# Kernel optimization log

Measured on AMD Instinct MI355X. Metric: run time of the kernel, lower is better.

The kernel has to match this reference:

```python
import jax, jax.numpy as jnp
import numpy as np

H = 16
D_MODEL = 1024
D_K = D_MODEL // H
SEQ = 2048
BATCH = 2


def setup_inputs() -> dict:
    key = jax.random.key(0)
    ks = jax.random.split(key, 11)
    s = 1.0 / np.sqrt(D_MODEL)
    inp = {
        "query": jax.random.normal(ks[0], (SEQ, BATCH, D_MODEL), jnp.float32),
        "key_": jax.random.normal(ks[1], (SEQ, BATCH, D_MODEL), jnp.float32),
        "value": jax.random.normal(ks[2], (SEQ, BATCH, D_MODEL), jnp.float32),
        "Wq": jax.random.uniform(ks[3], (D_MODEL, D_MODEL), jnp.float32, -s, s),
        "bq": jax.random.uniform(ks[4], (D_MODEL,), jnp.float32, -s, s),
        "Wk": jax.random.uniform(ks[5], (D_MODEL, D_MODEL), jnp.float32, -s, s),
        "bk": jax.random.uniform(ks[6], (D_MODEL,), jnp.float32, -s, s),
        "Wv": jax.random.uniform(ks[7], (D_MODEL, D_MODEL), jnp.float32, -s, s),
        "bv": jax.random.uniform(ks[8], (D_MODEL,), jnp.float32, -s, s),
        "Wo": jax.random.uniform(ks[9], (D_MODEL, D_MODEL), jnp.float32, -s, s),
        "bo": jax.random.uniform(ks[10], (D_MODEL,), jnp.float32, -s, s),
    }
    return inp


def _mha(query, key_, value, Wq, bq, Wk, bk, Wv, bv, Wo, bo):
    S, B, D = query.shape
    # torch Linear: x @ W.T + b; then view(S,B,h,dk).transpose(0,2) -> [h,B,S,dk]
    def proj(x, W, b):
        return jnp.transpose((x @ W.T + b).reshape(S, B, H, D_K), (2, 1, 0, 3))

    q = proj(query, Wq, bq)   # [h, b, S, dk]
    k = proj(key_, Wk, bk)
    v = proj(value, Wv, bv)

    scores = jnp.einsum("hbqd,hbkd->hbqk", q, k) / jnp.sqrt(
        jnp.asarray(D_K, q.dtype)
    )  # [h, b, S, S]
    p_attn = jax.nn.softmax(scores, axis=-1)  # dropout p=0.0 -> identity
    x = jnp.einsum("hbqk,hbkd->hbqd", p_attn, v)  # [h, b, S, dk]
    x = jnp.transpose(x, (2, 1, 0, 3)).reshape(S, B, D)  # back to [S, B, D]
    return x @ Wo.T + bo


def reference(query, key_, value, Wq, bq, Wk, bk, Wv, bv, Wo, bo):
    return _mha(query, key_, value, Wq, bq, Wk, bk, Wv, bv, Wo, bo)
```

## Files before the change

### kernel.cpp

```cpp
#include <hip/hip_runtime.h>

#define SEQ   2048
#define BATCH 2
#define DM    1024
#define NH    16
#define DKD   64
#define MROWS (SEQ*BATCH)

#define QSCALE 0.18033688011112042f

using bf16x8 = __attribute__((ext_vector_type(8))) __bf16;
using bf16x4 = __attribute__((ext_vector_type(4))) __bf16;
using bf16x2 = __attribute__((ext_vector_type(2))) __bf16;
using f32x4  = __attribute__((ext_vector_type(4))) float;

__device__ __forceinline__ void gld_lds16(const __bf16* g, __bf16* l) {
  __builtin_amdgcn_global_load_lds(
      (__attribute__((address_space(1))) void*)(g),
      (__attribute__((address_space(3))) void*)(l), 16, 0, 0);
}

__global__ __launch_bounds__(256) void cvt_all(
    const float* __restrict__ s0, const float* __restrict__ s1,
    const float* __restrict__ s2, const float* __restrict__ s3,
    const float* __restrict__ s4, const float* __restrict__ s5,
    const float* __restrict__ s6,
    __bf16* __restrict__ d0, __bf16* __restrict__ d1, __bf16* __restrict__ d2,
    __bf16* __restrict__ d3, __bf16* __restrict__ d4, __bf16* __restrict__ d5,
    __bf16* __restrict__ d6, int n_big, int n_small) {
  int y = blockIdx.y;
  const float* s; __bf16* d;
  switch (y) {
    case 0: s = s0; d = d0; break;
    case 1: s = s1; d = d1; break;
    case 2: s = s2; d = d2; break;
    case 3: s = s3; d = d3; break;
    case 4: s = s4; d = d4; break;
    case 5: s = s5; d = d5; break;
    default: s = s6; d = d6; break;
  }
  int n = (y < 3) ? n_big : n_small;
  int i = (blockIdx.x * 256 + threadIdx.x) * 8;
  if (i >= n) return;
  const float4* sp = (const float4*)(s + i);
  float4 a = sp[0], b = sp[1];
  bf16x8 v;
  v[0]=(__bf16)a.x; v[1]=(__bf16)a.y; v[2]=(__bf16)a.z; v[3]=(__bf16)a.w;
  v[4]=(__bf16)b.x; v[5]=(__bf16)b.y; v[6]=(__bf16)b.z; v[7]=(__bf16)b.w;
  *(bf16x8*)(d + i) = v;
}

__device__ __forceinline__ void gemm_core(const __bf16* __restrict__ A,
                                          const __bf16* __restrict__ Bt,
                                          __bf16* Ash, __bf16* Bsh,
                                          f32x4 acc[4][4], int m0, int n0) {
  const int K = DM;
  int tid = threadIdx.x;
  int lane = tid & 63, quad = lane >> 4, l16 = lane & 15;
  int w = tid >> 6;
  int wm = (w & 1) * 64, wn = (w >> 1) * 64;
  for (int k0 = 0; k0 < K; k0 += 32) {
    __syncthreads();
#pragma unroll
    for (int it = 0; it < 2; ++it) {
      int c   = tid + it * 256;
      int row = c >> 2, ko = (c & 3) * 8;
      int base = (tid - lane + it * 256) * 8;
      gld_lds16(A  + (size_t)(m0 + row) * K + k0 + ko, Ash + base);
      gld_lds16(Bt + (size_t)(n0 + row) * K + k0 + ko, Bsh + base);
    }
    __syncthreads();
    bf16x8 af[4], bfr[4];
#pragma unroll
    for (int mi = 0; mi < 4; mi++)
      af[mi] = *(const bf16x8*)&Ash[(wm + mi * 16 + l16) * 32 + quad * 8];
#pragma unroll
    for (int ni = 0; ni < 4; ni++)
      bfr[ni] = *(const bf16x8*)&Bsh[(wn + ni * 16 + l16) * 32 + quad * 8];
#pragma unroll
    for (int mi = 0; mi < 4; mi++)
#pragma unroll
      for (int ni = 0; ni < 4; ni++)
        acc[mi][ni] = __builtin_amdgcn_mfma_f32_16x16x32_bf16(
            af[mi], bfr[ni], acc[mi][ni], 0, 0, 0);
  }
}

__global__ __launch_bounds__(256, 3) void gemm_qkv(
    const __bf16* __restrict__ Xq, const __bf16* __restrict__ Xk,
    const __bf16* __restrict__ Xv, const __bf16* __restrict__ Wqkv,
    const float* __restrict__ bqp, const float* __restrict__ bkp,
    const float* __restrict__ bvp,
    __bf16* __restrict__ Qb, __bf16* __restrict__ Kb, __bf16* __restrict__ Vt) {
  __shared__ __bf16 Ash[128 * 32], Bsh[128 * 32];
  __shared__ __bf16 Esh[4][16 * 72];
  int z = blockIdx.z;
  const __bf16* A   = (z == 0) ? Xq : (z == 1) ? Xk : Xv;
  const __bf16* Bt  = Wqkv + (size_t)z * (DM * DM);
  const float* bias = (z == 0) ? bqp : (z == 1) ? bkp : bvp;
  int m0 = blockIdx.y * 128, n0 = blockIdx.x * 128;
  f32x4 acc[4][4] = {};
  gemm_core(A, Bt, Ash, Bsh, acc, m0, n0);

  int tid = threadIdx.x, lane = tid & 63, quad = lane >> 4, l16 = lane & 15;
  int w = tid >> 6, wm = (w & 1) * 64, wn = (w >> 1) * 64;
  __bf16* E = Esh[w];
  int n_base = n0 + wn;
  int hh = n_base >> 6;
  float scale = (z == 0) ? QSCALE : 1.0f;
  float bb[4];
#pragma unroll
  for (int ni = 0; ni < 4; ni++) bb[ni] = bias[n_base + ni * 16 + l16] * scale;

  if (z == 2) {
#pragma unroll
    for (int ni = 0; ni < 4; ni++) {
#pragma unroll
      for (int mi = 0; mi < 4; mi++) {
        int s0 = mi * 8 + quad * 2;
        bf16x2 p0, p1;
        p0[0] = (__bf16)(acc[mi][ni][0] + bb[ni]);
        p0[1] = (__bf16)(acc[mi][ni][2] + bb[ni]);
        p1[0] = (__bf16)(acc[mi][ni][1] + bb[ni]);
        p1[1] = (__bf16)(acc[mi][ni][3] + bb[ni]);
        *(bf16x2*)&E[l16 * 72 + s0]      = p0;
        *(bf16x2*)&E[l16 * 72 + 32 + s0] = p1;
      }
      asm volatile("s_waitcnt lgkmcnt(0)" ::: "memory");
#pragma unroll
      for (int pass = 0; pass < 2; pass++) {
        int ddl = pass * 8 + (lane >> 3);
        int col = (lane & 7) * 8;
        bf16x8 v = *(const bf16x8*)&E[ddl * 72 + col];
        int b2 = col >> 5, sl = col & 31;
        int dd = ni * 16 + ddl;
        int sg = ((m0 + wm) >> 1) + sl;
        *(bf16x8*)&Vt[(((size_t)hh * BATCH + b2) * DKD + dd) * SEQ + sg] = v;
      }
      asm volatile("s_waitcnt lgkmcnt(0)" ::: "memory");
    }
  } else {
    __bf16* Out = (z == 0) ? Qb : Kb;
#pragma unroll
    for (int mi = 0; mi < 4; mi++) {
#pragma unroll
      for (int ni = 0; ni < 4; ni++)
#pragma unroll
        for (int r = 0; r < 4; r++)
          E[(quad * 4 + r) * 72 + ni * 16 + l16] =
              (__bf16)fmaf(acc[mi][ni][r], scale, bb[ni]);
      asm volatile("s_waitcnt lgkmcnt(0)" ::: "memory");
#pragma unroll
      for (int pass = 0; pass < 2; pass++) {
        int row16 = pass * 8 + (lane >> 3);
        int coll  = (lane & 7) * 8;
        bf16x8 v = *(const bf16x8*)&E[row16 * 72 + coll];
        int m = m0 + wm + mi * 16 + row16;
        int s = m >> 1, b2 = m & 1;
        *(bf16x8*)&Out[(((size_t)hh * BATCH + b2) * SEQ + s) * DKD + coll] = v;
      }
      asm volatile("s_waitcnt lgkmcnt(0)" ::: "memory");
    }
  }
}

__global__ __launch_bounds__(256, 3) void gemm_out(
    const __bf16* __restrict__ A, const __bf16* __restrict__ Bt,
    const float* __restrict__ bias, float* __restrict__ out) {
  __shared__ __bf16 Ash[64 * 32], Bsh[128 * 32];
  const int K = DM;
  int m0 = blockIdx.y * 64, n0 = blockIdx.x * 128;
  int tid = threadIdx.x;
  int lane = tid & 63, quad = lane >> 4, l16 = lane & 15;
  int w = tid >> 6;
  int wm = (w & 1) * 32, wn = (w >> 1) * 64;
  f32x4 acc[2][4] = {};
  for (int k0 = 0; k0 < K; k0 += 32) {
    __syncthreads();
    {
      int c = tid;
      int row = c >> 2, ko = (c & 3) * 8;
      gld_lds16(A + (size_t)(m0 + row) * K + k0 + ko,
                Ash + (tid - lane) * 8);
    }
#pragma unroll
    for (int it = 0; it < 2; ++it) {
      int c = tid + it * 256;
      int row = c >> 2, ko = (c & 3) * 8;
      gld_lds16(Bt + (size_t)(n0 + row) * K + k0 + ko,
                Bsh + (tid - lane + it * 256) * 8);
    }
    __syncthreads();
    bf16x8 af[2], bfr[4];
#pragma unroll
    for (int mi = 0; mi < 2; mi++)
      af[mi] = *(const bf16x8*)&Ash[(wm + mi * 16 + l16) * 32 + quad * 8];
#pragma unroll
    for (int ni = 0; ni < 4; ni++)
      bfr[ni] = *(const bf16x8*)&Bsh[(wn + ni * 16 + l16) * 32 + quad * 8];
#pragma unroll
    for (int mi = 0; mi < 2; mi++)
#pragma unroll
      for (int ni = 0; ni < 4; ni++)
        acc[mi][ni] = __builtin_amdgcn_mfma_f32_16x16x32_bf16(
            af[mi], bfr[ni], acc[mi][ni], 0, 0, 0);
  }
#pragma unroll
  for (int ni = 0; ni < 4; ni++) {
    int n = n0 + wn + ni * 16 + l16;
    float bb = bias[n];
#pragma unroll
    for (int mi = 0; mi < 2; mi++) {
#pragma unroll
      for (int r = 0; r < 4; r++) {
        int m = m0 + wm + mi * 16 + quad * 4 + r;
        out[(size_t)m * DM + n] = acc[mi][ni][r] + bb;
      }
    }
  }
}

__global__ __launch_bounds__(256, 2) void flash_attn(
    const __bf16* __restrict__ Qg, const __bf16* __restrict__ Kg,
    const __bf16* __restrict__ Vtg, __bf16* __restrict__ Xa) {
  __shared__ __bf16 Ksh[2][64 * 64];
  __shared__ __bf16 Vsh[2][64 * 64];
  __shared__ __bf16 Psh[4][32 * 64];
  int tid = threadIdx.x, w = tid >> 6, lane = tid & 63;
  int quad = lane >> 4, l16 = lane & 15, sw = l16 & 7;
  int n = blockIdx.x;
  int hb = n & 31, qi = n >> 5;
  int h = hb >> 1, b = hb & 1, q0 = qi * 128;
  size_t hboff = ((size_t)h * BATCH + b) * SEQ * DKD;
  const __bf16* Qp = Qg + hboff;
  const __bf16* Kp = Kg + hboff;
  const __bf16* Vp = Vtg + hboff;
  __bf16* Pw = Psh[w];

  bf16x8 qf[2][2];
#pragma unroll
  for (int qb = 0; qb < 2; qb++)
#pragma unroll
    for (int kk = 0; kk < 2; kk++)
      qf[qb][kk] = *(const bf16x8*)(
          Qp + (size_t)(q0 + w * 32 + qb * 16 + l16) * DKD + kk * 32 + quad * 8);

  f32x4 o[2][4] = {};
  float l_[2] = {0.f, 0.f};

#pragma unroll
  for (int it = 0; it < 2; ++it) {
    int c = tid + it * 256;
    int r = c >> 3, pp = c & 7;
    int off = (pp ^ (r & 7)) << 3;
    gld_lds16(Kp + (size_t)r * DKD + off, Ksh[0] + c * 8);
    gld_lds16(Vp + (size_t)r * SEQ + off, Vsh[0] + c * 8);
  }

  for (int t = 0; t < SEQ / 64; ++t) {
    __syncthreads();
    if (t + 1 < SEQ / 64) {
      int k0n = (t + 1) * 64, bn = (t + 1) & 1;
#pragma unroll
      for (int it = 0; it < 2; ++it) {
        int c = tid + it * 256;
        int r = c >> 3, pp = c & 7;
        int off = (pp ^ (r & 7)) << 3;
        gld_lds16(Kp + (size_t)(k0n + r) * DKD + off, Ksh[bn] + c * 8);
        gld_lds16(Vp + (size_t)r * SEQ + k0n + off, Vsh[bn] + c * 8);
      }
    }
    const __bf16* Kb_ = Ksh[t & 1];
    const __bf16* Vb_ = Vsh[t & 1];

    f32x4 sc[2][4];
#pragma unroll
    for (int ji = 0; ji < 4; ji++) {
      int rr = ji * 16 + l16;
      bf16x8 kf0 = *(const bf16x8*)&Kb_[rr * 64 + ((quad ^ sw) << 3)];
      bf16x8 kf1 = *(const bf16x8*)&Kb_[rr * 64 + (((4 + quad) ^ sw) << 3)];
#pragma unroll
      for (int qb = 0; qb < 2; qb++) {
        f32x4 t2 = {0.f, 0.f, 0.f, 0.f};
        t2 = __builtin_amdgcn_mfma_f32_16x16x32_bf16(kf0, qf[qb][0], t2, 0, 0, 0);
        t2 = __builtin_amdgcn_mfma_f32_16x16x32_bf16(kf1, qf[qb][1], t2, 0, 0, 0);
        sc[qb][ji] = t2;
      }
    }

#pragma unroll
    for (int qb = 0; qb < 2; qb++) {
#pragma unroll
      for (int ji = 0; ji < 4; ji++) {
        bf16x4 pk;
#pragma unroll
        for (int r = 0; r < 4; r++) {
          float pv = exp2f(sc[qb][ji][r]);
          l_[qb] += pv;
          pk[r] = (__bf16)pv;
        }
        *(bf16x4*)&Pw[(qb * 16 + l16) * 64 +
                      (((ji * 2 + (quad >> 1)) ^ sw) << 3) + ((quad & 1) << 2)] = pk;
      }
    }

#pragma unroll
    for (int kk = 0; kk < 2; kk++) {
      bf16x8 pa[2];
#pragma unroll
      for (int qb = 0; qb < 2; qb++)
        pa[qb] = *(const bf16x8*)&Pw[(qb * 16 + l16) * 64 +
                                     (((kk * 4 + quad) ^ sw) << 3)];
#pragma unroll
      for (int ni = 0; ni < 4; ni++) {
        int rr = ni * 16 + l16;
        bf16x8 vb = *(const bf16x8*)&Vb_[rr * 64 + (((kk * 4 + quad) ^ sw) << 3)];
#pragma unroll
        for (int qb = 0; qb < 2; qb++)
          o[qb][ni] = __builtin_amdgcn_mfma_f32_16x16x32_bf16(pa[qb], vb,
                                                              o[qb][ni], 0, 0, 0);
      }
    }
  }

#pragma unroll
  for (int qb = 0; qb < 2; qb++) {
    l_[qb] += __shfl_xor(l_[qb], 16, 64);
    l_[qb] += __shfl_xor(l_[qb], 32, 64);
    l_[qb] = 1.0f / l_[qb];
  }
#pragma unroll
  for (int qb = 0; qb < 2; qb++)
#pragma unroll
    for (int r = 0; r < 4; r++) {
      float li = __shfl(l_[qb], quad * 4 + r, 64);
      int q = q0 + w * 32 + qb * 16 + quad * 4 + r;
#pragma unroll
      for (int ni = 0; ni < 4; ni++) {
        int d = ni * 16 + l16;
        Xa[((size_t)q * BATCH + b) * DM + h * DKD + d] =
            (__bf16)(o[qb][ni][r] * li);
      }
    }
}

extern "C" void kernel_launch(void* const* d_in, const int* in_sizes, int n_in,
                              void* d_out, int out_size, void* d_ws,
                              size_t ws_size, hipStream_t stream) {
  (void)in_sizes; (void)n_in; (void)out_size; (void)ws_size;
  const float* query = (const float*)d_in[0];
  const float* key_  = (const float*)d_in[1];
  const float* value = (const float*)d_in[2];
  const float* Wq = (const float*)d_in[3];
  const float* bq = (const float*)d_in[4];
  const float* Wk = (const float*)d_in[5];
  const float* bk = (const float*)d_in[6];
  const float* Wv = (const float*)d_in[7];
  const float* bv = (const float*)d_in[8];
  const float* Wo = (const float*)d_in[9];
  const float* bo = (const float*)d_in[10];

  const size_t NX = (size_t)MROWS * DM;
  const size_t NW = (size_t)DM * DM;
  __bf16* p    = (__bf16*)d_ws;
  __bf16* Xq   = p; p += NX;
  __bf16* Xk   = p; p += NX;
  __bf16* Xv   = p; p += NX;
  __bf16* Wqkv = p; p += 3 * NW;
  __bf16* Wob  = p; p += NW;
  __bf16* Qb   = p; p += NX;
  __bf16* Kb   = p; p += NX;
  __bf16* Vt   = p; p += NX;
  __bf16* Xa   = Xq;

  cvt_all<<<dim3((unsigned)(NX / 2048), 7), 256, 0, stream>>>(
      query, key_, value, Wq, Wk, Wv, Wo,
      Xq, Xk, Xv, Wqkv, Wqkv + NW, Wqkv + 2 * NW, Wob, (int)NX, (int)NW);

  gemm_qkv<<<dim3(DM / 128, MROWS / 128, 3), 256, 0, stream>>>(
      Xq, Xk, Xv, Wqkv, bq, bk, bv, Qb, Kb, Vt);
  flash_attn<<<dim3(512), 256, 0, stream>>>(Qb, Kb, Vt, Xa);
  gemm_out<<<dim3(DM / 128, MROWS / 64), 256, 0, stream>>>(
      Xa, Wob, bo, (float*)d_out);
}
```

Baseline: 234.8 us.

## Use 8 waves of 16 query rows per flash-attention block

The flash-attention block now launches 512 threads (8 waves) instead of 256, and each wave handles 16 query rows instead of 32. Each thread also loads one K/V chunk per tile instead of two. This cuts per-thread registers and raises wave-level parallelism and latency hiding, but K and V fragments read from LDS are reused across half as many queries per wave, which doubles LDS read traffic per MFMA.

```diff
diff --git a/kernel.cpp b/kernel.cpp
--- a/kernel.cpp
+++ b/kernel.cpp
@@ -220,12 +220,12 @@
   }
 }
 
-__global__ __launch_bounds__(256, 2) void flash_attn(
+__global__ __launch_bounds__(512, 4) void flash_attn(
     const __bf16* __restrict__ Qg, const __bf16* __restrict__ Kg,
     const __bf16* __restrict__ Vtg, __bf16* __restrict__ Xa) {
   __shared__ __bf16 Ksh[2][64 * 64];
   __shared__ __bf16 Vsh[2][64 * 64];
-  __shared__ __bf16 Psh[4][32 * 64];
+  __shared__ __bf16 Psh[8][16 * 64];
   int tid = threadIdx.x, w = tid >> 6, lane = tid & 63;
   int quad = lane >> 4, l16 = lane & 15, sw = l16 & 7;
   int n = blockIdx.x;
@@ -237,20 +237,17 @@
   const __bf16* Vp = Vtg + hboff;
   __bf16* Pw = Psh[w];
 
-  bf16x8 qf[2][2];
-#pragma unroll
-  for (int qb = 0; qb < 2; qb++)
-#pragma unroll
-    for (int kk = 0; kk < 2; kk++)
-      qf[qb][kk] = *(const bf16x8*)(
-          Qp + (size_t)(q0 + w * 32 + qb * 16 + l16) * DKD + kk * 32 + quad * 8);
-
-  f32x4 o[2][4] = {};
-  float l_[2] = {0.f, 0.f};
-
-#pragma unroll
-  for (int it = 0; it < 2; ++it) {
-    int c = tid + it * 256;
+  bf16x8 qf[2];
+#pragma unroll
+  for (int kk = 0; kk < 2; kk++)
+    qf[kk] = *(const bf16x8*)(
+        Qp + (size_t)(q0 + w * 16 + l16) * DKD + kk * 32 + quad * 8);
+
+  f32x4 o[4] = {};
+  float l_ = 0.f;
+
+  {
+    int c = tid;
     int r = c >> 3, pp = c & 7;
     int off = (pp ^ (r & 7)) << 3;
     gld_lds16(Kp + (size_t)r * DKD + off, Ksh[0] + c * 8);
@@ -261,87 +258,66 @@
     __syncthreads();
     if (t + 1 < SEQ / 64) {
       int k0n = (t + 1) * 64, bn = (t + 1) & 1;
-#pragma unroll
-      for (int it = 0; it < 2; ++it) {
-        int c = tid + it * 256;
-        int r = c >> 3, pp = c & 7;
-        int off = (pp ^ (r & 7)) << 3;
-        gld_lds16(Kp + (size_t)(k0n + r) * DKD + off, Ksh[bn] + c * 8);
-        gld_lds16(Vp + (size_t)r * SEQ + k0n + off, Vsh[bn] + c * 8);
-      }
+      int c = tid;
+      int r = c >> 3, pp = c & 7;
+      int off = (pp ^ (r & 7)) << 3;
+      gld_lds16(Kp + (size_t)(k0n + r) * DKD + off, Ksh[bn] + c * 8);
+      gld_lds16(Vp + (size_t)r * SEQ + k0n + off, Vsh[bn] + c * 8);
     }
     const __bf16* Kb_ = Ksh[t & 1];
     const __bf16* Vb_ = Vsh[t & 1];
 
-    f32x4 sc[2][4];
+    f32x4 sc[4];
 #pragma unroll
     for (int ji = 0; ji < 4; ji++) {
       int rr = ji * 16 + l16;
       bf16x8 kf0 = *(const bf16x8*)&Kb_[rr * 64 + ((quad ^ sw) << 3)];
       bf16x8 kf1 = *(const bf16x8*)&Kb_[rr * 64 + (((4 + quad) ^ sw) << 3)];
-#pragma unroll
-      for (int qb = 0; qb < 2; qb++) {
-        f32x4 t2 = {0.f, 0.f, 0.f, 0.f};
-        t2 = __builtin_amdgcn_mfma_f32_16x16x32_bf16(kf0, qf[qb][0], t2, 0, 0, 0);
-        t2 = __builtin_amdgcn_mfma_f32_16x16x32_bf16(kf1, qf[qb][1], t2, 0, 0, 0);
-        sc[qb][ji] = t2;
-      }
-    }
-
-#pragma unroll
-    for (int qb = 0; qb < 2; qb++) {
-#pragma unroll
-      for (int ji = 0; ji < 4; ji++) {
-        bf16x4 pk;
-#pragma unroll
-        for (int r = 0; r < 4; r++) {
-          float pv = exp2f(sc[qb][ji][r]);
-          l_[qb] += pv;
-          pk[r] = (__bf16)pv;
-        }
-        *(bf16x4*)&Pw[(qb * 16 + l16) * 64 +
-                      (((ji * 2 + (quad >> 1)) ^ sw) << 3) + ((quad & 1) << 2)] = pk;
-      }
+      f32x4 t2 = {0.f, 0.f, 0.f, 0.f};
+      t2 = __builtin_amdgcn_mfma_f32_16x16x32_bf16(kf0, qf[0], t2, 0, 0, 0);
+      t2 = __builtin_amdgcn_mfma_f32_16x16x32_bf16(kf1, qf[1], t2, 0, 0, 0);
+      sc[ji] = t2;
+    }
+
+#pragma unroll
+    for (int ji = 0; ji < 4; ji++) {
+      bf16x4 pk;
+#pragma unroll
+      for (int r = 0; r < 4; r++) {
+        float pv = exp2f(sc[ji][r]);
+        l_ += pv;
+        pk[r] = (__bf16)pv;
+      }
+      *(bf16x4*)&Pw[l16 * 64 +
+                    (((ji * 2 + (quad >> 1)) ^ sw) << 3) + ((quad & 1) << 2)] = pk;
     }
 
 #pragma unroll
     for (int kk = 0; kk < 2; kk++) {
-      bf16x8 pa[2];
-#pragma unroll
-      for (int qb = 0; qb < 2; qb++)
-        pa[qb] = *(const bf16x8*)&Pw[(qb * 16 + l16) * 64 +
-                                     (((kk * 4 + quad) ^ sw) << 3)];
+      bf16x8 pa = *(const bf16x8*)&Pw[l16 * 64 + (((kk * 4 + quad) ^ sw) << 3)];
 #pragma unroll
       for (int ni = 0; ni < 4; ni++) {
         int rr = ni * 16 + l16;
         bf16x8 vb = *(const bf16x8*)&Vb_[rr * 64 + (((kk * 4 + quad) ^ sw) << 3)];
-#pragma unroll
-        for (int qb = 0; qb < 2; qb++)
-          o[qb][ni] = __builtin_amdgcn_mfma_f32_16x16x32_bf16(pa[qb], vb,
-                                                              o[qb][ni], 0, 0, 0);
-      }
-    }
-  }
-
-#pragma unroll
-  for (int qb = 0; qb < 2; qb++) {
-    l_[qb] += __shfl_xor(l_[qb], 16, 64);
-    l_[qb] += __shfl_xor(l_[qb], 32, 64);
-    l_[qb] = 1.0f / l_[qb];
-  }
-#pragma unroll
-  for (int qb = 0; qb < 2; qb++)
-#pragma unroll
-    for (int r = 0; r < 4; r++) {
-      float li = __shfl(l_[qb], quad * 4 + r, 64);
-      int q = q0 + w * 32 + qb * 16 + quad * 4 + r;
-#pragma unroll
-      for (int ni = 0; ni < 4; ni++) {
-        int d = ni * 16 + l16;
-        Xa[((size_t)q * BATCH + b) * DM + h * DKD + d] =
-            (__bf16)(o[qb][ni][r] * li);
-      }
-    }
+        o[ni] = __builtin_amdgcn_mfma_f32_16x16x32_bf16(pa, vb, o[ni], 0, 0, 0);
+      }
+    }
+  }
+
+  l_ += __shfl_xor(l_, 16, 64);
+  l_ += __shfl_xor(l_, 32, 64);
+  l_ = 1.0f / l_;
+#pragma unroll
+  for (int r = 0; r < 4; r++) {
+    float li = __shfl(l_, quad * 4 + r, 64);
+    int q = q0 + w * 16 + quad * 4 + r;
+#pragma unroll
+    for (int ni = 0; ni < 4; ni++) {
+      int d = ni * 16 + l16;
+      Xa[((size_t)q * BATCH + b) * DM + h * DKD + d] =
+          (__bf16)(o[ni][r] * li);
+    }
+  }
 }
 
 extern "C" void kernel_launch(void* const* d_in, const int* in_sizes, int n_in,
@@ -379,7 +355,7 @@
 
   gemm_qkv<<<dim3(DM / 128, MROWS / 128, 3), 256, 0, stream>>>(
       Xq, Xk, Xv, Wqkv, bq, bk, bv, Qb, Kb, Vt);
-  flash_attn<<<dim3(512), 256, 0, stream>>>(Qb, Kb, Vt, Xa);
+  flash_attn<<<dim3(512), 512, 0, stream>>>(Qb, Kb, Vt, Xa);
   gemm_out<<<dim3(DM / 128, MROWS / 64), 256, 0, stream>>>(
       Xa, Wob, bo, (float*)d_out);
 }
```

Result: faster. 228.6 us (-2.6%).
